# Performance work log

Measured on AMD Instinct MI355X. Metric: run time of the kernel, lower is better.

The kernel has to match this reference:

```python
import jax, jax.numpy as jnp
import numpy as np

B, C, H, W = 2, 128, 64, 64  # in_channels == mlp_dim == 128 (residual requires equality)
MLP = 128


def setup_inputs() -> dict:
    key = jax.random.key(0)
    ks = jax.random.split(key, 12)
    s = 1.0 / np.sqrt(C)
    inp = {
        "x": jax.random.normal(ks[0], (B, C, H, W), jnp.float32),
        "y": jax.random.normal(ks[1], (B, C, H, W), jnp.float32),
        # stacked params for the 4 TransLayers: [4, out, in] weights, [4, out] biases
        "Wq": jax.random.uniform(ks[2], (4, MLP, C), jnp.float32, -s, s),
        "bq": jax.random.uniform(ks[3], (4, MLP), jnp.float32, -s, s),
        "Wk": jax.random.uniform(ks[4], (4, MLP, C), jnp.float32, -s, s),
        "bk": jax.random.uniform(ks[5], (4, MLP), jnp.float32, -s, s),
        "Wv": jax.random.uniform(ks[6], (4, MLP, C), jnp.float32, -s, s),
        "bv": jax.random.uniform(ks[7], (4, MLP), jnp.float32, -s, s),
        "Wo": jax.random.uniform(ks[8], (4, MLP, C), jnp.float32, -s, s),
        "bo": jax.random.uniform(ks[9], (4, MLP), jnp.float32, -s, s),
    }
    return inp


def _conv1x1_relu(x, w, b):
    # x: [B,C,H,W], w: [O,C], b: [O]  -> [B,O,H,W]
    return jax.nn.relu(jnp.einsum('bchw,oc->bohw', x, w) + b[None, :, None, None])


def _trans_layer(x, y, wq, bq, wk, bk, wv, bv, wo, bo):
    Q = _conv1x1_relu(x, wq, bq)  # [B,C,H,W]
    K = _conv1x1_relu(y, wk, bk)
    V = _conv1x1_relu(y, wv, bv)
    b, c, h, w = Q.shape
    n = h * w
    Qf = Q.reshape(b, c, n).transpose(0, 2, 1)  # [B,N,C]
    Kf = K.reshape(b, c, n)                      # [B,C,N]
    Vf = V.reshape(b, c, n).transpose(0, 2, 1)   # [B,N,C]
    attn = jax.nn.softmax(jnp.einsum('bnc,bcm->bnm', Qf, Kf), axis=-1)  # unscaled, [B,N,N]
    wV = jnp.einsum('bnm,bmc->bnc', attn, Vf)    # [B,N,C]
    wV = wV.transpose(0, 2, 1).reshape(b, c, h, w)
    return _conv1x1_relu(wV, wo, bo) + x


def reference(x, y, Wq, bq, Wk, bk, Wv, bv, Wo, bo):
    layer = lambda i, a, b_: _trans_layer(a, b_, Wq[i], bq[i], Wk[i], bk[i],
                                          Wv[i], bv[i], Wo[i], bo[i])
    fuse_xy = layer(0, x, y)
    fuse_yz = layer(1, y, x)
    fuse_xx = layer(2, fuse_xy, fuse_xy)
    fuse_yy = layer(3, fuse_yz, fuse_yz)
    return fuse_xx + fuse_yy
```

## Files before the change

### kernel.cpp

```cpp
#include <hip/hip_runtime.h>
#include <math.h>

#define C 128
#define NSP 4096
#define LOG2E 1.4426950408889634f

typedef __attribute__((ext_vector_type(8))) short short8;
typedef __attribute__((ext_vector_type(4))) float f32x4;
typedef __attribute__((ext_vector_type(16))) float f32x16;

static __device__ __forceinline__ unsigned short f2bf(float f) {
    union { float f; unsigned u; } a; a.f = f;
    unsigned r = a.u + 0x7fffu + ((a.u >> 16) & 1u);
    return (unsigned short)(r >> 16);
}

static __device__ __forceinline__ float bf2f(unsigned short s) {
    union { unsigned u; float f; } a; a.u = (unsigned)s << 16;
    return a.f;
}

static __device__ __forceinline__ unsigned pkbf(float a, float b) {
    union { float f; unsigned u; } ua, ub; ua.f = a; ub.f = b;
    return __builtin_amdgcn_perm(ub.u + 0x8000u, ua.u + 0x8000u, 0x07060302u);
}

static __device__ __forceinline__ float ex2(float x) {
#if __has_builtin(__builtin_amdgcn_exp2f)
    return __builtin_amdgcn_exp2f(x);
#else
    return exp2f(x);
#endif
}

static __device__ __forceinline__ f32x4 mfma16(short8 a, short8 b, f32x4 c) {
    return __builtin_amdgcn_mfma_f32_16x16x32_bf16(a, b, c, 0, 0, 0);
}

static __device__ __forceinline__ f32x16 mfma32(short8 a, short8 b, f32x16 c) {
    return __builtin_amdgcn_mfma_f32_32x32x16_bf16(a, b, c, 0, 0, 0);
}

static __device__ __forceinline__ void stage_w(const float* __restrict__ W,
                                               unsigned short* __restrict__ Wl, int t,
                                               float scale) {
#pragma unroll
    for (int i = 0; i < 16; i++) {
        int idx = i * 256 + t;
        int o = idx >> 5, c4 = (idx & 31) << 2;
        float4 v = *reinterpret_cast<const float4*>(W + o * C + c4);
        uint2 u;
        u.x = pkbf(v.x * scale, v.y * scale);
        u.y = pkbf(v.z * scale, v.w * scale);
        *reinterpret_cast<uint2*>(&Wl[o * 136 + c4]) = u;
    }
}

static __device__ __forceinline__ void stage_in(const float* __restrict__ In, int n0,
                                                unsigned short* __restrict__ Il, int t) {
#pragma unroll
    for (int i = 0; i < 8; i++) {
        int idx = i * 256 + t;
        int c = idx >> 4, n4 = (idx & 15) << 2;
        float4 v = *reinterpret_cast<const float4*>(In + (size_t)c * NSP + n0 + n4);
        Il[(n4 + 0) * 136 + c] = f2bf(v.x);
        Il[(n4 + 1) * 136 + c] = f2bf(v.y);
        Il[(n4 + 2) * 136 + c] = f2bf(v.z);
        Il[(n4 + 3) * 136 + c] = f2bf(v.w);
    }
}

static __device__ __forceinline__ void stage_nc(const unsigned short* __restrict__ In, int n0,
                                                unsigned short* __restrict__ Il, int t) {
#pragma unroll
    for (int i = 0; i < 4; i++) {
        int idx = i * 256 + t;
        int n = idx >> 4, c8 = (idx & 15) << 3;
        uint4 v = *reinterpret_cast<const uint4*>(In + (size_t)(n0 + n) * C + c8);
        *reinterpret_cast<uint4*>(&Il[n * 136 + c8]) = v;
    }
}

__global__ __launch_bounds__(256)
void qkv_kernel(const float* __restrict__ qs0, const float* __restrict__ qs1,
                const float* __restrict__ kv0, const float* __restrict__ kv1,
                const float* __restrict__ Wq, const float* __restrict__ Wk,
                const float* __restrict__ Wv,
                const float* __restrict__ bq, const float* __restrict__ bk,
                const float* __restrict__ bv,
                int layer_base,
                unsigned short* __restrict__ Qb, unsigned short* __restrict__ Kb,
                unsigned short* __restrict__ Vb)
{
    __shared__ __align__(16) unsigned short Wl[128 * 136];
    __shared__ __align__(16) unsigned short Il[64 * 136];
    const int t = threadIdx.x;
    const int ntile = blockIdx.x, kind = blockIdx.y, jb = blockIdx.z;
    const int job = jb >> 1, b = jb & 1, layer = layer_base + job;
    const float* src = (kind == 0) ? (job ? qs1 : qs0) : (job ? kv1 : kv0);
    const float* In = src + (size_t)b * C * NSP;
    const float* W = ((kind == 0) ? Wq : (kind == 1) ? Wk : Wv) + (size_t)layer * C * C;
    const float* bias = ((kind == 0) ? bq : (kind == 1) ? bk : bv) + layer * C;
    unsigned short* Out = ((kind == 0) ? Qb : (kind == 1) ? Kb : Vb) + (size_t)jb * NSP * C;
    const float scale = (kind == 0) ? LOG2E : 1.0f;
    const int n0 = ntile * 64;

    stage_w(W, Wl, t, scale);
    stage_in(In, n0, Il, t);
    __syncthreads();

    const int lane = t & 63, w = t >> 6, l15 = lane & 15, quad = lane >> 4;

    if (kind <= 1) {
        f32x4 acc[4][2];
#pragma unroll
        for (int nt = 0; nt < 4; nt++)
#pragma unroll
            for (int ot = 0; ot < 2; ot++)
#pragma unroll
                for (int r = 0; r < 4; r++) acc[nt][ot][r] = 0.0f;
#pragma unroll
        for (int ks = 0; ks < 4; ks++) {
            int co = ks * 32 + quad * 8;
            short8 b0 = *reinterpret_cast<const short8*>(&Wl[(w * 32 + l15) * 136 + co]);
            short8 b1 = *reinterpret_cast<const short8*>(&Wl[(w * 32 + 16 + l15) * 136 + co]);
#pragma unroll
            for (int nt = 0; nt < 4; nt++) {
                short8 a = *reinterpret_cast<const short8*>(&Il[(nt * 16 + l15) * 136 + co]);
                acc[nt][0] = mfma16(a, b0, acc[nt][0]);
                acc[nt][1] = mfma16(a, b1, acc[nt][1]);
            }
        }
        float bz0 = bias[w * 32 + l15] * scale;
        float bz1 = bias[w * 32 + 16 + l15] * scale;
#pragma unroll
        for (int nt = 0; nt < 4; nt++)
#pragma unroll
            for (int ot = 0; ot < 2; ot++)
#pragma unroll
                for (int r = 0; r < 4; r++) {
                    float v = fmaxf(acc[nt][ot][r] + (ot ? bz1 : bz0), 0.0f);
                    int n = n0 + nt * 16 + quad * 4 + r;
                    int o = w * 32 + ot * 16 + l15;
                    Out[(size_t)n * C + o] = f2bf(v);
                }
    } else {
        f32x4 acc[2][4];
#pragma unroll
        for (int ot = 0; ot < 2; ot++)
#pragma unroll
            for (int nt = 0; nt < 4; nt++)
#pragma unroll
                for (int r = 0; r < 4; r++) acc[ot][nt][r] = 0.0f;
#pragma unroll
        for (int ks = 0; ks < 4; ks++) {
            int co = ks * 32 + quad * 8;
            short8 a0 = *reinterpret_cast<const short8*>(&Wl[(w * 32 + l15) * 136 + co]);
            short8 a1 = *reinterpret_cast<const short8*>(&Wl[(w * 32 + 16 + l15) * 136 + co]);
#pragma unroll
            for (int nt = 0; nt < 4; nt++) {
                short8 bb = *reinterpret_cast<const short8*>(&Il[(nt * 16 + l15) * 136 + co]);
                acc[0][nt] = mfma16(a0, bb, acc[0][nt]);
                acc[1][nt] = mfma16(a1, bb, acc[1][nt]);
            }
        }
#pragma unroll
        for (int ot = 0; ot < 2; ot++)
#pragma unroll
            for (int r = 0; r < 4; r++) {
                int o = w * 32 + ot * 16 + quad * 4 + r;
                float bz = bias[o];
#pragma unroll
                for (int nt = 0; nt < 4; nt++) {
                    float v = fmaxf(acc[ot][nt][r] + bz, 0.0f);
                    Out[(size_t)o * NSP + n0 + nt * 16 + l15] = f2bf(v);
                }
            }
    }
}

__global__ __launch_bounds__(512)
void attn_kernel(const unsigned short* __restrict__ Qb, const unsigned short* __restrict__ Kb,
                 const unsigned short* __restrict__ Vb, unsigned short* __restrict__ Op,
                 float* __restrict__ Lp, int iters)
{
    __shared__ __align__(16) unsigned short Kl[2][32 * 136];
    __shared__ __align__(16) unsigned short Vl[2][128 * 40];
    const int t = threadIdx.x, lane = t & 63, w = t >> 6;
    const int l31 = lane & 31, hi = lane >> 5;

    const int ksz = gridDim.z;
    const int nwg = gridDim.x * gridDim.y * ksz;
    const int linear = blockIdx.x + gridDim.x * (blockIdx.y + gridDim.y * blockIdx.z);
    const int cpx = nwg >> 3;
    const int wid = (linear & 7) * cpx + (linear >> 3);
    const int ntile = wid & 15;
    const int r2 = wid >> 4;
    const int jb = r2 / ksz, kc = r2 % ksz;

    const int n0 = ntile * 256 + w * 32;
    const int m_begin = kc * iters * 32;
    const unsigned short* Q = Qb + (size_t)jb * NSP * C;
    const unsigned short* K = Kb + (size_t)jb * NSP * C;
    const unsigned short* V = Vb + (size_t)jb * NSP * C;

    short8 qf[8];
#pragma unroll
    for (int ks = 0; ks < 8; ks++)
        qf[ks] = *reinterpret_cast<const short8*>(
            Q + (size_t)(n0 + l31) * C + ks * 16 + hi * 8);

    f32x16 o_acc[4];
#pragma unroll
    for (int ct = 0; ct < 4; ct++)
#pragma unroll
        for (int r = 0; r < 16; r++) o_acc[ct][r] = 0.0f;
    float L = 0.0f;

    uint4 kreg, vreg;
    const int km_ = t >> 4, kc8_ = (t & 15) << 3;
    const int vc_ = t >> 2, vm8_ = (t & 3) << 3;

#define ATT_LOAD(BLK)                                                                  \
    {                                                                                  \
        int mb_ = m_begin + (BLK) * 32;                                                \
        kreg = *reinterpret_cast<const uint4*>(K + (size_t)(mb_ + km_) * C + kc8_);    \
        vreg = *reinterpret_cast<const uint4*>(V + (size_t)vc_ * NSP + mb_ + vm8_);    \
    }

#define ATT_STORE(BUF)                                                                 \
    {                                                                                  \
        *reinterpret_cast<uint4*>(&Kl[BUF][km_ * 136 + kc8_]) = kreg;                  \
        *reinterpret_cast<uint4*>(&Vl[BUF][vc_ * 40 + vm8_]) = vreg;                   \
    }

    ATT_LOAD(0);
    ATT_STORE(0);
    if (iters > 1) ATT_LOAD(1);
    __syncthreads();

    int cur = 0;
    for (int blk = 0; blk < iters; blk++) {
        const unsigned short* Kc = &Kl[cur][0];
        const unsigned short* Vc = &Vl[cur][0];

        f32x16 s;
#pragma unroll
        for (int r = 0; r < 16; r++) s[r] = 0.0f;
        __builtin_amdgcn_s_setprio(1);
#pragma unroll
        for (int ks = 0; ks < 8; ks++) {
            short8 ka = *reinterpret_cast<const short8*>(&Kc[l31 * 136 + ks * 16 + hi * 8]);
            s = mfma32(ka, qf[ks], s);
        }
        __builtin_amdgcn_s_setprio(0);

        if (blk + 1 < iters) {
            ATT_STORE(cur ^ 1);
            if (blk + 2 < iters) ATT_LOAD(blk + 2);
        }

        float p[16];
        float ls = 0.0f;
#pragma unroll
        for (int r = 0; r < 16; r++) {
            p[r] = ex2(s[r]);
            ls += p[r];
        }
        L += ls;

        unsigned a0 = pkbf(p[0], p[1]),  a1 = pkbf(p[2], p[3]);
        unsigned b0 = pkbf(p[4], p[5]),  b1 = pkbf(p[6], p[7]);
        unsigned c0 = pkbf(p[8], p[9]),  c1 = pkbf(p[10], p[11]);
        unsigned d0 = pkbf(p[12], p[13]), d1 = pkbf(p[14], p[15]);
        asm("v_permlane32_swap_b32 %0, %1" : "+v"(a0), "+v"(b0));
        asm("v_permlane32_swap_b32 %0, %1" : "+v"(a1), "+v"(b1));
        asm("v_permlane32_swap_b32 %0, %1" : "+v"(c0), "+v"(d0));
        asm("v_permlane32_swap_b32 %0, %1" : "+v"(c1), "+v"(d1));
        union { uint4 u; short8 s8; } f0u, f1u;
        f0u.u = make_uint4(a0, a1, b0, b1);
        f1u.u = make_uint4(c0, c1, d0, d1);

        __builtin_amdgcn_s_setprio(1);
#pragma unroll
        for (int ct = 0; ct < 4; ct++) {
            short8 v0 = *reinterpret_cast<const short8*>(&Vc[(ct * 32 + l31) * 40 + hi * 8]);
            short8 v1 = *reinterpret_cast<const short8*>(&Vc[(ct * 32 + l31) * 40 + 16 + hi * 8]);
            o_acc[ct] = mfma32(v0, f0u.s8, o_acc[ct]);
            o_acc[ct] = mfma32(v1, f1u.s8, o_acc[ct]);
        }
        __builtin_amdgcn_s_setprio(0);

        __syncthreads();
        cur ^= 1;
    }

#undef ATT_LOAD
#undef ATT_STORE

    const size_t kjb = (size_t)(kc * 4 + jb);
    float Lv = L + __shfl_xor(L, 32);
    if (lane < 32) Lp[kjb * NSP + n0 + l31] = Lv;

    unsigned short* Ob = Op + kjb * NSP * C;
    const int n = n0 + l31;
    unsigned short* On = Ob + (size_t)n * C + hi * 4;
#pragma unroll
    for (int ct = 0; ct < 4; ct++)
#pragma unroll
        for (int rb = 0; rb < 4; rb++) {
            int r0 = rb * 4;
            uint2 u;
            u.x = pkbf(o_acc[ct][r0 + 0], o_acc[ct][r0 + 1]);
            u.y = pkbf(o_acc[ct][r0 + 2], o_acc[ct][r0 + 3]);
            *reinterpret_cast<uint2*>(On + ct * 32 + rb * 8) = u;
        }
}

__global__ __launch_bounds__(256)
void combine_kernel(unsigned short* __restrict__ Op, const float* __restrict__ Lp, int nks)
{
    int gid = blockIdx.x * 256 + threadIdx.x;
    int c8 = (gid & 15) << 3;
    int n  = (gid >> 4) & 4095;
    int jb = gid >> 16;
    float Ls = 0.0f;
    for (int k = 0; k < nks; k++) Ls += Lp[(size_t)(k * 4 + jb) * NSP + n];
    float o[8];
#pragma unroll
    for (int j = 0; j < 8; j++) o[j] = 0.0f;
    for (int k = 0; k < nks; k++) {
        union { uint4 v; unsigned short s[8]; } u;
        u.v = *reinterpret_cast<const uint4*>(Op + ((size_t)(k * 4 + jb) * NSP + n) * C + c8);
#pragma unroll
        for (int j = 0; j < 8; j++) o[j] += bf2f(u.s[j]);
    }
    float inv = 1.0f / Ls;
    uint4 r;
    r.x = pkbf(o[0] * inv, o[1] * inv);
    r.y = pkbf(o[2] * inv, o[3] * inv);
    r.z = pkbf(o[4] * inv, o[5] * inv);
    r.w = pkbf(o[6] * inv, o[7] * inv);
    *reinterpret_cast<uint4*>(Op + ((size_t)jb * NSP + n) * C + c8) = r;
}

__global__ __launch_bounds__(256)
void proj_kernel(const unsigned short* __restrict__ att, const float* __restrict__ Wo,
                 const float* __restrict__ bo, int layer_base,
                 const float* __restrict__ res0, const float* __restrict__ res1,
                 float* __restrict__ out0, float* __restrict__ out1)
{
    __shared__ __align__(16) unsigned short Wl[128 * 136];
    __shared__ __align__(16) unsigned short Il[64 * 136];
    const int t = threadIdx.x;
    const int ntile = blockIdx.x, jb = blockIdx.y;
    const int job = jb >> 1, b = jb & 1, layer = layer_base + job;
    const unsigned short* In = att + (size_t)jb * NSP * C;
    const float* bias = bo + layer * C;
    const float* res = (job ? res1 : res0) + (size_t)b * C * NSP;
    float* out = (job ? out1 : out0) + (size_t)b * C * NSP;
    const int n0 = ntile * 64;

    stage_w(Wo + (size_t)layer * C * C, Wl, t, 1.0f);
    stage_nc(In, n0, Il, t);
    __syncthreads();

    const int lane = t & 63, w = t >> 6, l15 = lane & 15, quad = lane >> 4;
    f32x4 acc[2][4];
#pragma unroll
    for (int ot = 0; ot < 2; ot++)
#pragma unroll
        for (int nt = 0; nt < 4; nt++)
#pragma unroll
            for (int r = 0; r < 4; r++) acc[ot][nt][r] = 0.0f;
#pragma unroll
    for (int ks = 0; ks < 4; ks++) {
        int co = ks * 32 + quad * 8;
        short8 a0 = *reinterpret_cast<const short8*>(&Wl[(w * 32 + l15) * 136 + co]);
        short8 a1 = *reinterpret_cast<const short8*>(&Wl[(w * 32 + 16 + l15) * 136 + co]);
#pragma unroll
        for (int nt = 0; nt < 4; nt++) {
            short8 bb = *reinterpret_cast<const short8*>(&Il[(nt * 16 + l15) * 136 + co]);
            acc[0][nt] = mfma16(a0, bb, acc[0][nt]);
            acc[1][nt] = mfma16(a1, bb, acc[1][nt]);
        }
    }
#pragma unroll
    for (int ot = 0; ot < 2; ot++)
#pragma unroll
        for (int r = 0; r < 4; r++) {
            int o = w * 32 + ot * 16 + quad * 4 + r;
            float bz = bias[o];
#pragma unroll
            for (int nt = 0; nt < 4; nt++) {
                int n = n0 + nt * 16 + l15;
                float v = fmaxf(acc[ot][nt][r] + bz, 0.0f) + res[(size_t)o * NSP + n];
                out[(size_t)o * NSP + n] = v;
            }
        }
}

__global__ __launch_bounds__(256)
void final_kernel(const unsigned short* __restrict__ att, const float* __restrict__ Wo,
                  const float* __restrict__ bo,
                  const float* __restrict__ fuse0, const float* __restrict__ fuse1,
                  float* __restrict__ out)
{
    __shared__ __align__(16) unsigned short Wl[128 * 136];
    __shared__ __align__(16) unsigned short Il[64 * 136];
    const int t = threadIdx.x;
    const int ntile = blockIdx.x, b = blockIdx.y;
    const int n0 = ntile * 64;
    const int lane = t & 63, w = t >> 6, l15 = lane & 15, quad = lane >> 4;

    float tot[2][4][4];
#pragma unroll
    for (int ot = 0; ot < 2; ot++)
#pragma unroll
        for (int nt = 0; nt < 4; nt++)
#pragma unroll
            for (int r = 0; r < 4; r++) tot[ot][nt][r] = 0.0f;

    for (int j = 0; j < 2; j++) {
        if (j) __syncthreads();
        int layer = 2 + j;
        stage_w(Wo + (size_t)layer * C * C, Wl, t, 1.0f);
        stage_nc(att + (size_t)(j * 2 + b) * NSP * C, n0, Il, t);
        __syncthreads();

        f32x4 acc[2][4];
#pragma unroll
        for (int ot = 0; ot < 2; ot++)
#pragma unroll
            for (int nt = 0; nt < 4; nt++)
#pragma unroll
                for (int r = 0; r < 4; r++) acc[ot][nt][r] = 0.0f;
#pragma unroll
        for (int ks = 0; ks < 4; ks++) {
            int co = ks * 32 + quad * 8;
            short8 a0 = *reinterpret_cast<const short8*>(&Wl[(w * 32 + l15) * 136 + co]);
            short8 a1 = *reinterpret_cast<const short8*>(&Wl[(w * 32 + 16 + l15) * 136 + co]);
#pragma unroll
            for (int nt = 0; nt < 4; nt++) {
                short8 bb = *reinterpret_cast<const short8*>(&Il[(nt * 16 + l15) * 136 + co]);
                acc[0][nt] = mfma16(a0, bb, acc[0][nt]);
                acc[1][nt] = mfma16(a1, bb, acc[1][nt]);
            }
        }
        const float* bias = bo + layer * C;
        const float* fuse = (j ? fuse1 : fuse0) + (size_t)b * C * NSP;
#pragma unroll
        for (int ot = 0; ot < 2; ot++)
#pragma unroll
            for (int r = 0; r < 4; r++) {
                int o = w * 32 + ot * 16 + quad * 4 + r;
                float bz = bias[o];
#pragma unroll
                for (int nt = 0; nt < 4; nt++) {
                    int n = n0 + nt * 16 + l15;
                    tot[ot][nt][r] += fmaxf(acc[ot][nt][r] + bz, 0.0f) + fuse[(size_t)o * NSP + n];
                }
            }
    }
#pragma unroll
    for (int ot = 0; ot < 2; ot++)
#pragma unroll
        for (int r = 0; r < 4; r++) {
            int o = w * 32 + ot * 16 + quad * 4 + r;
#pragma unroll
            for (int nt = 0; nt < 4; nt++) {
                int n = n0 + nt * 16 + l15;
                out[(size_t)b * C * NSP + (size_t)o * NSP + n] = tot[ot][nt][r];
            }
        }
}

extern "C" void kernel_launch(void* const* d_in, const int* in_sizes, int n_in,
                              void* d_out, int out_size, void* d_ws, size_t ws_size,
                              hipStream_t stream)
{
    (void)in_sizes; (void)n_in; (void)out_size;
    const float* x  = (const float*)d_in[0];
    const float* y  = (const float*)d_in[1];
    const float* Wq = (const float*)d_in[2];
    const float* bq = (const float*)d_in[3];
    const float* Wk = (const float*)d_in[4];
    const float* bk = (const float*)d_in[5];
    const float* Wv = (const float*)d_in[6];
    const float* bv = (const float*)d_in[7];
    const float* Wo = (const float*)d_in[8];
    const float* bo = (const float*)d_in[9];
    float* out = (float*)d_out;
    char* ws = (char*)d_ws;

    int ks = (ws_size >= 55050240u) ? 8 : (ws_size >= 38010880u) ? 4 : 2;
    int iters = 128 / ks;

    unsigned short* Qb = (unsigned short*)(ws);
    unsigned short* Kb = (unsigned short*)(ws + (4u << 20));
    unsigned short* Vb = (unsigned short*)(ws + (8u << 20));
    unsigned short* Op = (unsigned short*)(ws + (12u << 20));
    size_t op_bytes = (size_t)ks * 4 * NSP * C * 2;
    float* Lp = (float*)(ws + (12u << 20) + op_bytes);
    float* fuse0 = Lp + (size_t)ks * 4 * NSP;
    float* fuse1 = fuse0 + (size_t)2 * C * NSP;
    unsigned short* att = Op;

    qkv_kernel<<<dim3(64, 3, 4), 256, 0, stream>>>(x, y, y, x, Wq, Wk, Wv, bq, bk, bv, 0,
                                                   Qb, Kb, Vb);
    attn_kernel<<<dim3(16, 4, ks), 512, 0, stream>>>(Qb, Kb, Vb, Op, Lp, iters);
    combine_kernel<<<dim3(1024), 256, 0, stream>>>(Op, Lp, ks);
    proj_kernel<<<dim3(64, 4), 256, 0, stream>>>(att, Wo, bo, 0, x, y, fuse0, fuse1);

    qkv_kernel<<<dim3(64, 3, 4), 256, 0, stream>>>(fuse0, fuse1, fuse0, fuse1, Wq, Wk, Wv,
                                                   bq, bk, bv, 2, Qb, Kb, Vb);
    attn_kernel<<<dim3(16, 4, ks), 512, 0, stream>>>(Qb, Kb, Vb, Op, Lp, iters);
    combine_kernel<<<dim3(1024), 256, 0, stream>>>(Op, Lp, ks);
    final_kernel<<<dim3(64, 2), 256, 0, stream>>>(att, Wo, bo, fuse0, fuse1, out);
}
```

Before: 223.5 us.

## Fuse split-K attention combine into output projection kernels

Removes the separate combine kernel and folds the split-K reduction (sum of partial outputs and normalisers, then normalise) into the staging step of the projection and final kernels. This drops two kernel launches and one write/read round trip of the combined attention tensor. It also sets a minimum-occupancy launch bound on the attention kernel and reuses the score registers for probabilities to ease register pressure. The trade-off is that the projection kernels, which have small grids, now do the reduction reads themselves with less parallelism.

New measurement: 257.2 us. 1.15x slower.

```diff
diff --git a/kernel.cpp b/kernel.cpp
--- a/kernel.cpp
+++ b/kernel.cpp
@@ -70,14 +70,33 @@
     }
 }
 
-static __device__ __forceinline__ void stage_nc(const unsigned short* __restrict__ In, int n0,
-                                                unsigned short* __restrict__ Il, int t) {
+static __device__ __forceinline__ void stage_sum(const unsigned short* __restrict__ Op,
+                                                 const float* __restrict__ Lp,
+                                                 int jb, int nks, int n0,
+                                                 unsigned short* __restrict__ Il, int t) {
 #pragma unroll
     for (int i = 0; i < 4; i++) {
         int idx = i * 256 + t;
         int n = idx >> 4, c8 = (idx & 15) << 3;
-        uint4 v = *reinterpret_cast<const uint4*>(In + (size_t)(n0 + n) * C + c8);
-        *reinterpret_cast<uint4*>(&Il[n * 136 + c8]) = v;
+        float o[8];
+#pragma unroll
+        for (int j = 0; j < 8; j++) o[j] = 0.0f;
+        float Ls = 0.0f;
+        for (int k = 0; k < nks; k++) {
+            size_t kjb = (size_t)(k * 4 + jb);
+            Ls += Lp[kjb * NSP + n0 + n];
+            union { uint4 v; unsigned short s[8]; } u;
+            u.v = *reinterpret_cast<const uint4*>(Op + (kjb * NSP + n0 + n) * C + c8);
+#pragma unroll
+            for (int j = 0; j < 8; j++) o[j] += bf2f(u.s[j]);
+        }
+        float inv = 1.0f / Ls;
+        union { uint4 v; unsigned u[4]; } w;
+        w.u[0] = pkbf(o[0] * inv, o[1] * inv);
+        w.u[1] = pkbf(o[2] * inv, o[3] * inv);
+        w.u[2] = pkbf(o[4] * inv, o[5] * inv);
+        w.u[3] = pkbf(o[6] * inv, o[7] * inv);
+        *reinterpret_cast<uint4*>(&Il[n * 136 + c8]) = w.v;
     }
 }
 
@@ -179,14 +198,14 @@
     }
 }
 
-__global__ __launch_bounds__(512)
+__global__ __launch_bounds__(512, 4)
 void attn_kernel(const unsigned short* __restrict__ Qb, const unsigned short* __restrict__ Kb,
                  const unsigned short* __restrict__ Vb, unsigned short* __restrict__ Op,
                  float* __restrict__ Lp, int iters)
 {
     __shared__ __align__(16) unsigned short Kl[2][32 * 136];
     __shared__ __align__(16) unsigned short Vl[2][128 * 40];
-    const int t = threadIdx.x, lane = t & 63, w = t >> 6;
+    const int t = threadIdx.x, lane = t & 63;
     const int l31 = lane & 31, hi = lane >> 5;
 
     const int ksz = gridDim.z;
@@ -198,7 +217,7 @@
     const int r2 = wid >> 4;
     const int jb = r2 / ksz, kc = r2 % ksz;
 
-    const int n0 = ntile * 256 + w * 32;
+    const int n0 = ntile * 256 + (t >> 6) * 32;
     const int m_begin = kc * iters * 32;
     const unsigned short* Q = Qb + (size_t)jb * NSP * C;
     const unsigned short* K = Kb + (size_t)jb * NSP * C;
@@ -260,19 +279,18 @@
             if (blk + 2 < iters) ATT_LOAD(blk + 2);
         }
 
-        float p[16];
         float ls = 0.0f;
 #pragma unroll
         for (int r = 0; r < 16; r++) {
-            p[r] = ex2(s[r]);
-            ls += p[r];
+            s[r] = ex2(s[r]);
+            ls += s[r];
         }
         L += ls;
 
-        unsigned a0 = pkbf(p[0], p[1]),  a1 = pkbf(p[2], p[3]);
-        unsigned b0 = pkbf(p[4], p[5]),  b1 = pkbf(p[6], p[7]);
-        unsigned c0 = pkbf(p[8], p[9]),  c1 = pkbf(p[10], p[11]);
-        unsigned d0 = pkbf(p[12], p[13]), d1 = pkbf(p[14], p[15]);
+        unsigned a0 = pkbf(s[0], s[1]),  a1 = pkbf(s[2], s[3]);
+        unsigned b0 = pkbf(s[4], s[5]),  b1 = pkbf(s[6], s[7]);
+        unsigned c0 = pkbf(s[8], s[9]),  c1 = pkbf(s[10], s[11]);
+        unsigned d0 = pkbf(s[12], s[13]), d1 = pkbf(s[14], s[15]);
         asm("v_permlane32_swap_b32 %0, %1" : "+v"(a0), "+v"(b0));
         asm("v_permlane32_swap_b32 %0, %1" : "+v"(a1), "+v"(b1));
         asm("v_permlane32_swap_b32 %0, %1" : "+v"(c0), "+v"(d0));
@@ -318,34 +336,8 @@
 }
 
 __global__ __launch_bounds__(256)
-void combine_kernel(unsigned short* __restrict__ Op, const float* __restrict__ Lp, int nks)
-{
-    int gid = blockIdx.x * 256 + threadIdx.x;
-    int c8 = (gid & 15) << 3;
-    int n  = (gid >> 4) & 4095;
-    int jb = gid >> 16;
-    float Ls = 0.0f;
-    for (int k = 0; k < nks; k++) Ls += Lp[(size_t)(k * 4 + jb) * NSP + n];
-    float o[8];
-#pragma unroll
-    for (int j = 0; j < 8; j++) o[j] = 0.0f;
-    for (int k = 0; k < nks; k++) {
-        union { uint4 v; unsigned short s[8]; } u;
-        u.v = *reinterpret_cast<const uint4*>(Op + ((size_t)(k * 4 + jb) * NSP + n) * C + c8);
-#pragma unroll
-        for (int j = 0; j < 8; j++) o[j] += bf2f(u.s[j]);
-    }
-    float inv = 1.0f / Ls;
-    uint4 r;
-    r.x = pkbf(o[0] * inv, o[1] * inv);
-    r.y = pkbf(o[2] * inv, o[3] * inv);
-    r.z = pkbf(o[4] * inv, o[5] * inv);
-    r.w = pkbf(o[6] * inv, o[7] * inv);
-    *reinterpret_cast<uint4*>(Op + ((size_t)jb * NSP + n) * C + c8) = r;
-}
-
-__global__ __launch_bounds__(256)
-void proj_kernel(const unsigned short* __restrict__ att, const float* __restrict__ Wo,
+void proj_kernel(const unsigned short* __restrict__ Op, const float* __restrict__ Lp, int nks,
+                 const float* __restrict__ Wo,
                  const float* __restrict__ bo, int layer_base,
                  const float* __restrict__ res0, const float* __restrict__ res1,
                  float* __restrict__ out0, float* __restrict__ out1)
@@ -355,14 +347,13 @@
     const int t = threadIdx.x;
     const int ntile = blockIdx.x, jb = blockIdx.y;
     const int job = jb >> 1, b = jb & 1, layer = layer_base + job;
-    const unsigned short* In = att + (size_t)jb * NSP * C;
     const float* bias = bo + layer * C;
     const float* res = (job ? res1 : res0) + (size_t)b * C * NSP;
     float* out = (job ? out1 : out0) + (size_t)b * C * NSP;
     const int n0 = ntile * 64;
 
     stage_w(Wo + (size_t)layer * C * C, Wl, t, 1.0f);
-    stage_nc(In, n0, Il, t);
+    stage_sum(Op, Lp, jb, nks, n0, Il, t);
     __syncthreads();
 
     const int lane = t & 63, w = t >> 6, l15 = lane & 15, quad = lane >> 4;
@@ -401,7 +392,8 @@
 }
 
 __global__ __launch_bounds__(256)
-void final_kernel(const unsigned short* __restrict__ att, const float* __restrict__ Wo,
+void final_kernel(const unsigned short* __restrict__ Op, const float* __restrict__ Lp, int nks,
+                  const float* __restrict__ Wo,
                   const float* __restrict__ bo,
                   const float* __restrict__ fuse0, const float* __restrict__ fuse1,
                   float* __restrict__ out)
@@ -425,7 +417,7 @@
         if (j) __syncthreads();
         int layer = 2 + j;
         stage_w(Wo + (size_t)layer * C * C, Wl, t, 1.0f);
-        stage_nc(att + (size_t)(j * 2 + b) * NSP * C, n0, Il, t);
+        stage_sum(Op, Lp, j * 2 + b, nks, n0, Il, t);
         __syncthreads();
 
         f32x4 acc[2][4];
@@ -504,17 +496,14 @@
     float* Lp = (float*)(ws + (12u << 20) + op_bytes);
     float* fuse0 = Lp + (size_t)ks * 4 * NSP;
     float* fuse1 = fuse0 + (size_t)2 * C * NSP;
-    unsigned short* att = Op;
 
     qkv_kernel<<<dim3(64, 3, 4), 256, 0, stream>>>(x, y, y, x, Wq, Wk, Wv, bq, bk, bv, 0,
                                                    Qb, Kb, Vb);
     attn_kernel<<<dim3(16, 4, ks), 512, 0, stream>>>(Qb, Kb, Vb, Op, Lp, iters);
-    combine_kernel<<<dim3(1024), 256, 0, stream>>>(Op, Lp, ks);
-    proj_kernel<<<dim3(64, 4), 256, 0, stream>>>(att, Wo, bo, 0, x, y, fuse0, fuse1);
+    proj_kernel<<<dim3(64, 4), 256, 0, stream>>>(Op, Lp, ks, Wo, bo, 0, x, y, fuse0, fuse1);
 
     qkv_kernel<<<dim3(64, 3, 4), 256, 0, stream>>>(fuse0, fuse1, fuse0, fuse1, Wq, Wk, Wv,
                                                    bq, bk, bv, 2, Qb, Kb, Vb);
     attn_kernel<<<dim3(16, 4, ks), 512, 0, stream>>>(Qb, Kb, Vb, Op, Lp, iters);
-    combine_kernel<<<dim3(1024), 256, 0, stream>>>(Op, Lp, ks);
-    final_kernel<<<dim3(64, 2), 256, 0, stream>>>(att, Wo, bo, fuse0, fuse1, out);
-}
+    final_kernel<<<dim3(64, 2), 256, 0, stream>>>(Op, Lp, ks, Wo, bo, fuse0, fuse1, out);
+}
```
